# Optimization experiments

Hardware: AMD Instinct MI355X
Metric: run time of the kernel (lower is better)

Reference implementation:

```python
import jax, jax.numpy as jnp
import numpy as np

TEMPERATURE = 0.1
B, T, D = 8, 1024, 1024
NEG_INF = -1e30

def setup_inputs() -> dict:
    key = jax.random.key(0)
    k1, k2, k3 = jax.random.split(key, 3)
    features = jax.random.normal(k1, (B, T, D), dtype=jnp.float32)
    masks = jax.random.bernoulli(k2, 0.05, (B, 1, T, T)).astype(jnp.float32)
    input_coords_length = jax.random.randint(k3, (B,), T // 2, T - 1)  # int32
    return {"features": features, "masks": masks, "input_coords_length": input_coords_length}


def _sup_con_loss(feat, mask, L):
    # feat: [T, D], mask: [T, T] float, L: scalar int valid length (slice [:L, :L])
    Tn = feat.shape[0]
    dt = feat.dtype
    vr = jnp.arange(Tn) < L                              # valid rows/cols [T]
    valid2d = (vr[:, None] & vr[None, :]).astype(dt)     # [T, T]
    dot = jnp.matmul(feat, feat.T) / TEMPERATURE         # [T, T]
    dot = jnp.where(vr[None, :], dot, NEG_INF)           # exclude padded cols from max
    logits = dot - jax.lax.stop_gradient(jnp.max(dot, axis=-1, keepdims=True))
    logits_mask = (1.0 - jnp.eye(Tn, dtype=dt)) * valid2d  # off-diagonal, in-slice
    exp_logits = jnp.exp(logits) * logits_mask
    m = mask * valid2d
    # negative_mask = 1-mask; entries < 1 zeroed (binary mask -> indicator of mask==0)
    neg = 1.0 - m
    neg = jnp.where(neg < 1.0, 0.0, neg) * valid2d
    # positive_mask = mask with entries > 0 set to 1
    pos = jnp.where(m > 0, 1.0, m)
    neg_denom = jnp.sum(exp_logits * neg, axis=-1, keepdims=True)
    pos_denom = jax.lax.stop_gradient(jnp.sum(exp_logits * pos, axis=-1, keepdims=True))
    log_prob = logits - jnp.log(neg_denom + pos_denom + 1e-6)
    m2 = m * logits_mask
    mean_log_prob_pos = (m2 * log_prob).sum(-1) / (m2.sum(-1) + 1e-6)  # [T]
    # mean over the L valid rows only (matches .mean() on the sliced tensor)
    return -jnp.sum(jnp.where(vr, mean_log_prob_pos, 0.0)) / L.astype(dt)


def _is_valid(mask, L):
    # valid sample iff sliced mask differs from eye(L) with [0,0]=0
    Tn = mask.shape[0]
    vr = jnp.arange(Tn) < L
    valid2d = (vr[:, None] & vr[None, :]).astype(mask.dtype)
    sanity = jnp.eye(Tn, dtype=mask.dtype).at[0, 0].set(0.0) * valid2d
    return jnp.any((mask * valid2d) != sanity)


def reference(features, masks, input_coords_length):
    L = input_coords_length + 1                      # [B]
    mask0 = masks[:, 0]                              # [B, T, T] (num_layers asserted == 1)
    losses = jax.vmap(_sup_con_loss)(features, mask0, L)   # [B]
    valid = jax.vmap(_is_valid)(mask0, L)                  # [B] bool
    vbs = jnp.maximum(jnp.sum(valid.astype(features.dtype)), 1.0)
    return jnp.sum(losses) / vbs
```

## Files before the change

kernel.cpp:

```cpp
#include <hip/hip_runtime.h>
#include <hip/hip_bf16.h>
#include <stdint.h>

#define T_DIM 1024
#define B_DIM 8

typedef __attribute__((ext_vector_type(8))) short short8;
typedef __attribute__((ext_vector_type(4))) float f32x4;

__device__ inline void gll16(const void* g, void* l) {
  __builtin_amdgcn_global_load_lds((__attribute__((address_space(1))) void*)g,
                                   (__attribute__((address_space(3))) void*)l,
                                   16, 0, 0);
}

__global__ __launch_bounds__(256) void convert_kernel(const float* __restrict__ F,
                                                      __hip_bfloat16* __restrict__ Fb) {
  const int t = blockIdx.x * 256 + threadIdx.x;
  const float4 v = ((const float4*)F)[t];
  union { __hip_bfloat16 h[4]; uint64_t u; } p;
  p.h[0] = __float2bfloat16(v.x);
  p.h[1] = __float2bfloat16(v.y);
  p.h[2] = __float2bfloat16(v.z);
  p.h[3] = __float2bfloat16(v.w);
  ((uint64_t*)Fb)[t] = p.u;
}

__global__ __launch_bounds__(512, 4) void fused_kernel(const __hip_bfloat16* __restrict__ Fb,
                                                       const float* __restrict__ M,
                                                       const int* __restrict__ icl,
                                                       float* __restrict__ part) {
  const int id = blockIdx.x;
  const int b  = id & 7;
  const int rt = (id >> 3) & 7;
  const int ct = id >> 6;
  const int L  = icl[b] + 1;
  if (rt * 128 >= L || ct * 128 >= L) return;

  __shared__ char smem[65536];
  __hip_bfloat16* As = (__hip_bfloat16*)smem;
  __hip_bfloat16* Bs = (__hip_bfloat16*)(smem + 32768);
  float* rp = (float*)smem;
  float* rp_m = rp;
  float* rp_d = rp + 512;
  float* rp_s = rp + 1024;
  float* rp_c = rp + 1536;
  float* rp_b = rp + 2048;

  const __hip_bfloat16* F = Fb + ((size_t)b << 20);
  const int tid  = threadIdx.x;
  const int lane = tid & 63;
  const int wave = tid >> 6;
  const int wrow = (wave >> 2) * 64;
  const int wcol = (wave & 3) * 32;
  const int row0 = rt * 128;
  const int col0 = ct * 128;

  const int fr = lane & 15;
  const int q  = lane >> 4;
  const int sl8 = (q ^ ((fr >> 1) & 3)) * 8;

  const int srow = tid >> 2;
  const int sgk  = (((tid & 3) ^ ((tid >> 3) & 3)) * 8);

  const int gc0 = col0 + wcol + fr;
  const int gc1 = gc0 + 16;

  float mv0[16], mv1[16];
  {
    const float* Mb = M + ((size_t)b << 20);
#pragma unroll
    for (int ti = 0; ti < 4; ti++)
#pragma unroll
      for (int r = 0; r < 4; r++) {
        const int grow = row0 + wrow + ti * 16 + q * 4 + r;
        const float* mrow = Mb + ((size_t)grow << 10);
        mv0[ti * 4 + r] = (gc0 < L) ? mrow[gc0] : 0.f;
        mv1[ti * 4 + r] = (gc1 < L) ? mrow[gc1] : 0.f;
      }
  }

  const size_t arow = (size_t)(row0 + srow) * T_DIM + sgk;
  const size_t brow = (size_t)(col0 + srow) * T_DIM + sgk;

  auto stage = [&](int buf, int step) {
    const int kb = step << 6;
#pragma unroll
    for (int p = 0; p < 2; p++)
      gll16(F + arow + kb + p * 32, As + buf * 8192 + p * 4096 + tid * 8);
#pragma unroll
    for (int p = 0; p < 2; p++)
      gll16(F + brow + kb + p * 32, Bs + buf * 8192 + p * 4096 + tid * 8);
  };

  stage(0, 0);
  stage(1, 1);

  uint32_t mbits = 0;
#pragma unroll
  for (int ti = 0; ti < 4; ti++)
#pragma unroll
    for (int r = 0; r < 4; r++) {
      const uint32_t b0 = (mv0[ti * 4 + r] != 0.f) ? 1u : 0u;
      const uint32_t b1 = (mv1[ti * 4 + r] != 0.f) ? 1u : 0u;
      mbits |= (b0 << (ti * 8 + r * 2)) | (b1 << (ti * 8 + r * 2 + 1));
    }

  f32x4 acc[4][2];
#pragma unroll
  for (int i = 0; i < 4; i++)
#pragma unroll
    for (int j = 0; j < 2; j++) acc[i][j] = (f32x4){0.f, 0.f, 0.f, 0.f};

#pragma unroll
  for (int t = 0; t < 16; ++t) {
    const int cur = t & 1;
    if (t < 15) { asm volatile("s_waitcnt vmcnt(4)" ::: "memory"); }
    else        { asm volatile("s_waitcnt vmcnt(0)" ::: "memory"); }
    __builtin_amdgcn_s_barrier();
    __builtin_amdgcn_sched_barrier(0);

    short8 af[2][4], bfr[2][2];
    const __hip_bfloat16* Ab = As + cur * 8192;
    const __hip_bfloat16* Bb = Bs + cur * 8192;
#pragma unroll
    for (int kk = 0; kk < 2; kk++) {
#pragma unroll
      for (int tt = 0; tt < 4; tt++)
        af[kk][tt] = *(const short8*)(Ab + kk * 4096 + (wrow + tt * 16 + fr) * 32 + sl8);
#pragma unroll
      for (int j = 0; j < 2; j++)
        bfr[kk][j] = *(const short8*)(Bb + kk * 4096 + (wcol + j * 16 + fr) * 32 + sl8);
    }
    asm volatile("s_waitcnt lgkmcnt(0)" ::: "memory");
    __builtin_amdgcn_sched_barrier(0);
    __builtin_amdgcn_s_barrier();
    __builtin_amdgcn_sched_barrier(0);

    if (t < 14) stage(cur, t + 2);

    __builtin_amdgcn_s_setprio(1);
#pragma unroll
    for (int kk = 0; kk < 2; kk++)
#pragma unroll
      for (int ti = 0; ti < 4; ti++)
#pragma unroll
        for (int tj = 0; tj < 2; tj++)
          acc[ti][tj] = __builtin_amdgcn_mfma_f32_16x16x32_bf16(af[kk][ti], bfr[kk][tj], acc[ti][tj], 0, 0, 0);
    __builtin_amdgcn_s_setprio(0);
  }
  __syncthreads();

#pragma unroll
  for (int ti = 0; ti < 4; ti++) {
#pragma unroll
    for (int r = 0; r < 4; r++) {
      const int lrow = wrow + ti * 16 + q * 4 + r;
      const int grow = row0 + lrow;
      const float mk0 = (float)((mbits >> (ti * 8 + r * 2)) & 1u);
      const float mk1 = (float)((mbits >> (ti * 8 + r * 2 + 1)) & 1u);
      const float s0 = (gc0 < L) ? acc[ti][0][r] * 10.0f : -1e30f;
      const float s1 = (gc1 < L) ? acc[ti][1][r] * 10.0f : -1e30f;
      float m = fmaxf(s0, s1);
#pragma unroll
      for (int d = 1; d < 16; d <<= 1) m = fmaxf(m, __shfl_xor(m, d, 64));
      float den = 0.f, msum = 0.f, cnt = 0.f, badf = 0.f;
      if (gc0 < L) {
        if (gc0 != grow) { den += __expf(s0 - m); msum += mk0 * s0; cnt += mk0; }
        const float sane = (gc0 == grow && grow != 0) ? 1.f : 0.f;
        badf = fmaxf(badf, (mk0 != sane) ? 1.f : 0.f);
      }
      if (gc1 < L) {
        if (gc1 != grow) { den += __expf(s1 - m); msum += mk1 * s1; cnt += mk1; }
        const float sane = (gc1 == grow && grow != 0) ? 1.f : 0.f;
        badf = fmaxf(badf, (mk1 != sane) ? 1.f : 0.f);
      }
#pragma unroll
      for (int d = 1; d < 16; d <<= 1) {
        den  += __shfl_xor(den, d, 64);
        msum += __shfl_xor(msum, d, 64);
        cnt  += __shfl_xor(cnt, d, 64);
        badf  = fmaxf(badf, __shfl_xor(badf, d, 64));
      }
      if (fr == 0) {
        const int slot = wave & 3;
        rp_m[lrow * 4 + slot] = m;   rp_d[lrow * 4 + slot] = den;
        rp_s[lrow * 4 + slot] = msum; rp_c[lrow * 4 + slot] = cnt;
        rp_b[lrow * 4 + slot] = badf;
      }
    }
  }
  __syncthreads();

  if (tid < 128) {
    float m = -1e30f;
#pragma unroll
    for (int s = 0; s < 4; s++) m = fmaxf(m, rp_m[tid * 4 + s]);
    float den = 0.f, msum = 0.f, cnt = 0.f, badf = 0.f;
#pragma unroll
    for (int s = 0; s < 4; s++) {
      den  += rp_d[tid * 4 + s] * __expf(rp_m[tid * 4 + s] - m);
      msum += rp_s[tid * 4 + s];
      cnt  += rp_c[tid * 4 + s];
      badf  = fmaxf(badf, rp_b[tid * 4 + s]);
    }
    float* p = part + ((((size_t)b * 1024 + row0 + tid) * 8) + ct) * 5;
    p[0] = m; p[1] = den; p[2] = msum; p[3] = cnt; p[4] = badf;
  }
}

__global__ __launch_bounds__(256) void reduce_kernel(const float* __restrict__ part,
                                                     const int* __restrict__ icl,
                                                     float* __restrict__ blk_sum,
                                                     int* __restrict__ blk_bad) {
  const int blk = blockIdx.x;
  const int row = blk * 256 + threadIdx.x;
  const int b = row >> 10;
  const int i = row & 1023;
  const int L = icl[b] + 1;
  float rv = 0.f;
  int bad = 0;
  if (i < L) {
    const float* p = part + (size_t)row * 40;
    const int ns = (L + 127) >> 7;
    float m = -1e30f;
    for (int s = 0; s < ns; s++) m = fmaxf(m, p[s * 5 + 0]);
    float den = 0.f, msum = 0.f, cnt = 0.f, badf = 0.f;
    for (int s = 0; s < ns; s++) {
      den  += p[s * 5 + 1] * __expf(p[s * 5 + 0] - m);
      msum += p[s * 5 + 2];
      cnt  += p[s * 5 + 3];
      badf  = fmaxf(badf, p[s * 5 + 4]);
    }
    const float A = msum - cnt * m;
    const float mlpp = (A - cnt * __logf(den + 1e-6f)) / (cnt + 1e-6f);
    rv = -mlpp / (float)L;
    bad = badf > 0.f ? 1 : 0;
  }
  const int tid  = threadIdx.x;
  const int lane = tid & 63;
  const int wave = tid >> 6;
  for (int o = 32; o > 0; o >>= 1) rv += __shfl_down(rv, o, 64);
  const int wbad = (__ballot(bad) != 0ull) ? 1 : 0;
  __shared__ float sred[4];
  __shared__ int bred[4];
  if (lane == 0) { sred[wave] = rv; bred[wave] = wbad; }
  __syncthreads();
  if (tid == 0) {
    blk_sum[blk] = sred[0] + sred[1] + sred[2] + sred[3];
    blk_bad[blk] = bred[0] | bred[1] | bred[2] | bred[3];
  }
}

__global__ __launch_bounds__(64) void final_kernel(const float* __restrict__ blk_sum,
                                                   const int* __restrict__ blk_bad,
                                                   float* __restrict__ out) {
  const int tid = threadIdx.x;
  float v = (tid < 32) ? blk_sum[tid] : 0.f;
  for (int o = 32; o > 0; o >>= 1) v += __shfl_down(v, o, 64);
  if (tid == 0) {
    int vcount = 0;
    for (int bb = 0; bb < B_DIM; bb++) {
      const int any = blk_bad[bb * 4] | blk_bad[bb * 4 + 1] |
                      blk_bad[bb * 4 + 2] | blk_bad[bb * 4 + 3];
      vcount += any ? 1 : 0;
    }
    out[0] = v / fmaxf((float)vcount, 1.0f);
  }
}

extern "C" void kernel_launch(void* const* d_in, const int* in_sizes, int n_in,
                              void* d_out, int out_size, void* d_ws, size_t ws_size,
                              hipStream_t stream) {
  const float* feat = (const float*)d_in[0];
  const float* mask = (const float*)d_in[1];
  const int*   icl  = (const int*)d_in[2];
  float* out = (float*)d_out;

  char* ws = (char*)d_ws;
  __hip_bfloat16* Fb = (__hip_bfloat16*)ws;
  float* part    = (float*)(ws + (16u << 20));
  float* blk_sum = (float*)(ws + (18u << 20));
  int*   blk_bad = (int*)(ws + (18u << 20) + 512);

  convert_kernel<<<dim3(8192), dim3(256), 0, stream>>>(feat, Fb);
  fused_kernel<<<dim3(512), dim3(512), 0, stream>>>(Fb, mask, icl, part);
  reduce_kernel<<<dim3(32), dim3(256), 0, stream>>>(part, icl, blk_sum, blk_bad);
  final_kernel<<<dim3(1), dim3(64), 0, stream>>>(blk_sum, blk_bad, out);
}
```

Before: 143.1 us.

## Transpose MFMA output layout so each lane holds contiguous row columns

Swaps the A/B operands of the MFMA so each lane owns four consecutive columns of one row instead of one column across four rows. The row-wise softmax reductions then run mostly in registers, and the cross-lane shuffle reductions shrink from 16 steps per row group to two xor steps per tile row. The mask is now read with float4 vector loads after the GEMM loop instead of scalar loads before it. This cuts global load instructions and register pressure during the main loop, but the mask load latency is no longer hidden behind the GEMM.

```diff
diff --git a/kernel.cpp b/kernel.cpp
--- a/kernel.cpp
+++ b/kernel.cpp
@@ -63,23 +63,6 @@
   const int srow = tid >> 2;
   const int sgk  = (((tid & 3) ^ ((tid >> 3) & 3)) * 8);
 
-  const int gc0 = col0 + wcol + fr;
-  const int gc1 = gc0 + 16;
-
-  float mv0[16], mv1[16];
-  {
-    const float* Mb = M + ((size_t)b << 20);
-#pragma unroll
-    for (int ti = 0; ti < 4; ti++)
-#pragma unroll
-      for (int r = 0; r < 4; r++) {
-        const int grow = row0 + wrow + ti * 16 + q * 4 + r;
-        const float* mrow = Mb + ((size_t)grow << 10);
-        mv0[ti * 4 + r] = (gc0 < L) ? mrow[gc0] : 0.f;
-        mv1[ti * 4 + r] = (gc1 < L) ? mrow[gc1] : 0.f;
-      }
-  }
-
   const size_t arow = (size_t)(row0 + srow) * T_DIM + sgk;
   const size_t brow = (size_t)(col0 + srow) * T_DIM + sgk;
 
@@ -95,16 +78,6 @@
 
   stage(0, 0);
   stage(1, 1);
-
-  uint32_t mbits = 0;
-#pragma unroll
-  for (int ti = 0; ti < 4; ti++)
-#pragma unroll
-    for (int r = 0; r < 4; r++) {
-      const uint32_t b0 = (mv0[ti * 4 + r] != 0.f) ? 1u : 0u;
-      const uint32_t b1 = (mv1[ti * 4 + r] != 0.f) ? 1u : 0u;
-      mbits |= (b0 << (ti * 8 + r * 2)) | (b1 << (ti * 8 + r * 2 + 1));
-    }
 
   f32x4 acc[4][2];
 #pragma unroll
@@ -146,48 +119,79 @@
       for (int ti = 0; ti < 4; ti++)
 #pragma unroll
         for (int tj = 0; tj < 2; tj++)
-          acc[ti][tj] = __builtin_amdgcn_mfma_f32_16x16x32_bf16(af[kk][ti], bfr[kk][tj], acc[ti][tj], 0, 0, 0);
+          acc[ti][tj] = __builtin_amdgcn_mfma_f32_16x16x32_bf16(bfr[kk][tj], af[kk][ti], acc[ti][tj], 0, 0, 0);
     __builtin_amdgcn_s_setprio(0);
   }
   __syncthreads();
 
+  uint32_t mbits = 0;
+  {
+    const float* Mb = M + ((size_t)b << 20);
+    union { float4 v; float f[4]; } mv[4][2];
+#pragma unroll
+    for (int ti = 0; ti < 4; ti++) {
+      const int grow = row0 + wrow + ti * 16 + fr;
+#pragma unroll
+      for (int tj = 0; tj < 2; tj++)
+        mv[ti][tj].v = *(const float4*)(Mb + ((size_t)grow << 10) + col0 + wcol + tj * 16 + q * 4);
+    }
+#pragma unroll
+    for (int ti = 0; ti < 4; ti++)
+#pragma unroll
+      for (int tj = 0; tj < 2; tj++)
+#pragma unroll
+        for (int r = 0; r < 4; r++)
+          mbits |= ((mv[ti][tj].f[r] != 0.f) ? 1u : 0u) << (ti * 8 + tj * 4 + r);
+  }
+
 #pragma unroll
   for (int ti = 0; ti < 4; ti++) {
-#pragma unroll
-    for (int r = 0; r < 4; r++) {
-      const int lrow = wrow + ti * 16 + q * 4 + r;
-      const int grow = row0 + lrow;
-      const float mk0 = (float)((mbits >> (ti * 8 + r * 2)) & 1u);
-      const float mk1 = (float)((mbits >> (ti * 8 + r * 2 + 1)) & 1u);
-      const float s0 = (gc0 < L) ? acc[ti][0][r] * 10.0f : -1e30f;
-      const float s1 = (gc1 < L) ? acc[ti][1][r] * 10.0f : -1e30f;
-      float m = fmaxf(s0, s1);
-#pragma unroll
-      for (int d = 1; d < 16; d <<= 1) m = fmaxf(m, __shfl_xor(m, d, 64));
-      float den = 0.f, msum = 0.f, cnt = 0.f, badf = 0.f;
-      if (gc0 < L) {
-        if (gc0 != grow) { den += __expf(s0 - m); msum += mk0 * s0; cnt += mk0; }
-        const float sane = (gc0 == grow && grow != 0) ? 1.f : 0.f;
-        badf = fmaxf(badf, (mk0 != sane) ? 1.f : 0.f);
+    const int lrow = wrow + ti * 16 + fr;
+    const int grow = row0 + lrow;
+    float s[2][4];
+#pragma unroll
+    for (int tj = 0; tj < 2; tj++)
+#pragma unroll
+      for (int r = 0; r < 4; r++) {
+        const int gcol = col0 + wcol + tj * 16 + q * 4 + r;
+        s[tj][r] = (gcol < L) ? acc[ti][tj][r] * 10.0f : -1e30f;
       }
-      if (gc1 < L) {
-        if (gc1 != grow) { den += __expf(s1 - m); msum += mk1 * s1; cnt += mk1; }
-        const float sane = (gc1 == grow && grow != 0) ? 1.f : 0.f;
-        badf = fmaxf(badf, (mk1 != sane) ? 1.f : 0.f);
+    float m = s[0][0];
+#pragma unroll
+    for (int tj = 0; tj < 2; tj++)
+#pragma unroll
+      for (int r = 0; r < 4; r++) m = fmaxf(m, s[tj][r]);
+    m = fmaxf(m, __shfl_xor(m, 16, 64));
+    m = fmaxf(m, __shfl_xor(m, 32, 64));
+
+    float den = 0.f, msum = 0.f, cnt = 0.f, badf = 0.f;
+#pragma unroll
+    for (int tj = 0; tj < 2; tj++)
+#pragma unroll
+      for (int r = 0; r < 4; r++) {
+        const int gcol = col0 + wcol + tj * 16 + q * 4 + r;
+        if (gcol < L) {
+          const float mk = (float)((mbits >> (ti * 8 + tj * 4 + r)) & 1u);
+          if (gcol != grow) {
+            den  += __expf(s[tj][r] - m);
+            msum += mk * s[tj][r];
+            cnt  += mk;
+          }
+          const float sane = (gcol == grow && grow != 0) ? 1.f : 0.f;
+          badf = fmaxf(badf, (mk != sane) ? 1.f : 0.f);
+        }
       }
-#pragma unroll
-      for (int d = 1; d < 16; d <<= 1) {
-        den  += __shfl_xor(den, d, 64);
-        msum += __shfl_xor(msum, d, 64);
-        cnt  += __shfl_xor(cnt, d, 64);
-        badf  = fmaxf(badf, __shfl_xor(badf, d, 64));
-      }
-      if (fr == 0) {
-        const int slot = wave & 3;
-        rp_m[lrow * 4 + slot] = m;   rp_d[lrow * 4 + slot] = den;
-        rp_s[lrow * 4 + slot] = msum; rp_c[lrow * 4 + slot] = cnt;
-        rp_b[lrow * 4 + slot] = badf;
-      }
+    den  += __shfl_xor(den, 16, 64);  den  += __shfl_xor(den, 32, 64);
+    msum += __shfl_xor(msum, 16, 64); msum += __shfl_xor(msum, 32, 64);
+    cnt  += __shfl_xor(cnt, 16, 64);  cnt  += __shfl_xor(cnt, 32, 64);
+    badf = fmaxf(badf, __shfl_xor(badf, 16, 64));
+    badf = fmaxf(badf, __shfl_xor(badf, 32, 64));
+
+    if (q == 0) {
+      const int slot = wave & 3;
+      rp_m[lrow * 4 + slot] = m;    rp_d[lrow * 4 + slot] = den;
+      rp_s[lrow * 4 + slot] = msum; rp_c[lrow * 4 + slot] = cnt;
+      rp_b[lrow * 4 + slot] = badf;
     }
   }
   __syncthreads();
```

Result: faster. 120.4 us (-15.9%).
